# Kernel tuning notes

Measured on AMD Instinct MI355X. Metric: run time of the kernel, lower is better.

## Reference

```python
import jax, jax.numpy as jnp
import numpy as np

LAYERS, BLOCKS = 10, 4
RC, DC, SC, EC = 32, 32, 256, 256  # residual, dilation, skip, end channels
CIN, COUT, K = 6, 1, 2
DILATIONS = [2 ** (i % LAYERS) for i in range(BLOCKS * LAYERS)]
NL = len(DILATIONS)


def conv1d(x, w, dilation=1, pad=0):
    # x: [N, C, T], w: [O, I, K]
    return jax.lax.conv_general_dilated(
        x, w, window_strides=(1,), padding=[(pad, pad)],
        rhs_dilation=(dilation,), dimension_numbers=('NCH', 'OIH', 'NCH'))


def setup_inputs() -> dict:
    key = jax.random.key(0)
    ks = jax.random.split(key, 10)
    s = 0.1
    return {
        'x': jax.random.normal(ks[0], (8, CIN, 8192), dtype=jnp.float32),
        'start_w': jax.random.normal(ks[1], (RC, CIN, 1), dtype=jnp.float32) * s,
        'filter_w': jax.random.normal(ks[2], (NL, DC, RC, K), dtype=jnp.float32) * s,
        'gate_w': jax.random.normal(ks[3], (NL, DC, RC, K), dtype=jnp.float32) * s,
        'res_w': jax.random.normal(ks[4], (NL, RC, DC, 1), dtype=jnp.float32) * s,
        'skip_w': jax.random.normal(ks[5], (NL, SC, DC, 1), dtype=jnp.float32) * s,
        'end1_w': jax.random.normal(ks[6], (EC, SC, 1), dtype=jnp.float32) * s,
        'end1_b': jax.random.normal(ks[7], (EC,), dtype=jnp.float32) * s,
        'end2_w': jax.random.normal(ks[8], (COUT, EC, 1), dtype=jnp.float32) * s,
        'end2_b': jax.random.normal(ks[9], (COUT,), dtype=jnp.float32) * s,
    }


def reference(x, start_w, filter_w, gate_w, res_w, skip_w, end1_w, end1_b, end2_w, end2_b):
    x = conv1d(x, start_w)  # [B, RC, T]
    T = x.shape[2]
    # symmetric padding=(K-1)*d makes length grow by d each layer;
    # the shortest skip is the first one: T + (K-1)*DILATIONS[0]
    min_len = T + (K - 1) * DILATIONS[0]
    skip_sum = jnp.zeros((x.shape[0], SC, min_len), dtype=x.dtype)
    for i, d in enumerate(DILATIONS):
        pad = (K - 1) * d
        f = jnp.tanh(conv1d(x, filter_w[i], d, pad))
        g = jax.nn.sigmoid(conv1d(x, gate_w[i], d, pad))
        x = f * g  # [B, DC, T'] with T' = T_prev + d
        s = conv1d(x, skip_w[i])
        skip_sum = skip_sum + s[:, :, -min_len:]
        x = conv1d(x, res_w[i]) + x  # residual add (RC == DC)
    h = jax.nn.relu(skip_sum)
    h = jax.nn.relu(conv1d(h, end1_w) + end1_b[None, :, None])
    h = conv1d(h, end2_w) + end2_b[None, :, None]
    return h[:, :, -1]  # [B, COUT]
```

## Files before the change

kernel.cpp:

```cpp
#include <hip/hip_runtime.h>
#include <hip/hip_fp16.h>
#include <math.h>


#define NL 40
#define TLEN 8192

#define F_BLOBFG 0
#define F_BLOBSK 40960
#define F_BLOBE1 204800
#define F_C0     237568

typedef __attribute__((ext_vector_type(2))) _Float16 h2;

#if defined(__has_builtin)
#if __has_builtin(__builtin_amdgcn_fdot2)
#define HAS_FDOT2 1
#endif
#endif

__device__ __forceinline__ float FDOT2(h2 a, h2 b, float c) {
#ifdef HAS_FDOT2
    return __builtin_amdgcn_fdot2(a, b, c, false);
#else
    return c + (float)a.x * (float)b.x + (float)a.y * (float)b.y;
#endif
}

__device__ __forceinline__ float tanh_fast(float f) {
    f = fminf(fmaxf(f, -15.f), 15.f);
    float e2 = __expf(2.f * f);
    return (e2 - 1.f) / (e2 + 1.f);
}

__global__ __launch_bounds__(256) void k1_prep(
    const float* __restrict__ x, const float* __restrict__ start_w,
    const float* __restrict__ filter_w, const float* __restrict__ gate_w,
    const float* __restrict__ res_w, const float* __restrict__ skip_w,
    const float* __restrict__ end1_w, float* __restrict__ ws)
{
    const int id = blockIdx.x, t = threadIdx.x;

    if (id < 80) {
        const int l = id >> 1, m = id & 1;
        __shared__ float F[32][32];
        __shared__ __align__(16) float R[32][36];
        const float* src = m ? gate_w : filter_w;
        for (int e = t; e < 1024; e += 256)
            F[e >> 5][e & 31] = src[(l * 1024 + e) * 2];
        if (l > 0)
            for (int e = t; e < 1024; e += 256) {
                const int k = e >> 5, j = e & 31;
                R[k][j] = res_w[(l - 1) * 1024 + e] + (k == j ? 1.f : 0.f);
            }
        __syncthreads();
        const int ch = t >> 3, jg = t & 7, j0 = jg * 4;
        float o0, o1, o2, o3;
        if (l == 0) {
            o0 = F[ch][j0]; o1 = F[ch][j0+1]; o2 = F[ch][j0+2]; o3 = F[ch][j0+3];
        } else {
            o0 = o1 = o2 = o3 = 0.f;
#pragma unroll
            for (int k = 0; k < 32; ++k) {
                const float fv = F[ch][k];
                const float4 rv = *(const float4*)&R[k][j0];
                o0 += fv*rv.x; o1 += fv*rv.y; o2 += fv*rv.z; o3 += fv*rv.w;
            }
        }
        const int hh = jg >> 2;
        __half* dst = (__half*)ws + (size_t)l * 2048 + (hh * 32 + ch) * 32
                    + (m ? 16 : 0) + (j0 & 15);
        ((__half2*)dst)[0] = __floats2half2_rn(o0, o1);
        ((__half2*)dst)[1] = __floats2half2_rn(o2, o3);
    }
    else if (id == 80) {
        const int b = t >> 5, ch = t & 31;
        float acc = 0.f;
#pragma unroll
        for (int j = 0; j < 6; ++j)
            acc += start_w[ch * 6 + j] * x[(b * 6 + j) * TLEN + TLEN - 1];
        ws[F_C0 + t] = acc;
    }
    else if (id < 241) {
        const int q = (id - 81) * 256 + t;
        const float4* s4 = (const float4*)skip_w;
        const float4 a = s4[q * 2], bb = s4[q * 2 + 1];
        __half2* d = (__half2*)(ws + F_BLOBSK);
        d[q * 4 + 0] = __floats2half2_rn(a.x,  a.y);
        d[q * 4 + 1] = __floats2half2_rn(a.z,  a.w);
        d[q * 4 + 2] = __floats2half2_rn(bb.x, bb.y);
        d[q * 4 + 3] = __floats2half2_rn(bb.z, bb.w);
    }
    else {
        __half2* d = (__half2*)(ws + F_BLOBE1);
#pragma unroll
        for (int k = 0; k < 2; ++k) {
            const int dd = (id - 241) * 512 + k * 256 + t;
            const int ec = dd & 255, sc2 = dd >> 8;
            const float v0 = end1_w[ec * 256 + 2 * sc2];
            const float v1 = end1_w[ec * 256 + 2 * sc2 + 1];
            d[dd] = __floats2half2_rn(v0, v1);
        }
    }
}

#define PF(L, W) do {                                                        \
    if ((L) < NL) {                                                          \
        _Pragma("unroll")                                                    \
        for (int i = 0; i < 4; ++i)                                          \
            W[i] = blobfg[(L) * 256 + lane * 4 + i];                         \
    }                                                                        \
} while (0)

#define SPF(L, SW) do {                                                      \
    if ((L) < NL) {                                                          \
        _Pragma("unroll")                                                    \
        for (int i = 0; i < 4; ++i)                                          \
            SW[i] = blobsk[(L) * 1024 + sc * 4 + i];                         \
    }                                                                        \
} while (0)

#define BODY(L, FG, SW) do {                                                 \
    if (wv == 0) {                                                           \
        h2 s[8];                                                             \
        { const float4* sp = (const float4*)zown;                            \
          *(float4*)&s[0] = sp[h * 2];                                       \
          *(float4*)&s[4] = sp[h * 2 + 1]; }                                 \
        float f = 0.f, g = 0.f;                                              \
        const h2* wfp = (const h2*)&FG[0];                                   \
        const h2* wgp = (const h2*)&FG[2];                                   \
        _Pragma("unroll")                                                    \
        for (int i = 0; i < 8; ++i) {                                        \
            f = FDOT2(wfp[i], s[i], f);                                      \
            g = FDOT2(wgp[i], s[i], g);                                      \
        }                                                                    \
        f += __shfl_xor(f, 32, 64);                                          \
        g += __shfl_xor(g, 32, 64);                                          \
        const float z = tanh_fast(f) * (1.f / (1.f + __expf(-g)));           \
        const __half hz = __float2half(z);                                   \
        if (h == 0) { zown[ch] = hz; zring[(L) & 1][ch] = hz; }              \
        PF((L) + 4, FG);                                                     \
    } else {                                                                 \
        if ((L) >= 1) {                                                      \
            const h2* zr2 = (const h2*)zring[((L) - 1) & 1];                 \
            const h2* wp  = (const h2*)SW;                                   \
            _Pragma("unroll")                                                \
            for (int i = 0; i < 16; ++i)                                     \
                skip_acc = FDOT2(wp[i], zr2[i], skip_acc);                   \
        }                                                                    \
        SPF((L) + 1, SW);                                                    \
    }                                                                        \
    __syncthreads();                                                         \
} while (0)

__global__ __launch_bounds__(320) void k2_all(
    const float* __restrict__ end1_b, const float* __restrict__ end2_w,
    const float* __restrict__ end2_b, const float* __restrict__ ws,
    float* __restrict__ out)
{
    const int b = blockIdx.x, t = threadIdx.x;
    const int wv = t >> 6, lane = t & 63;
    const int ch = lane & 31, h = lane >> 5;
    const int sc = t - 64;

    __shared__ __align__(16) __half zown[32];
    __shared__ __align__(16) __half zring[2][32];
    __shared__ __align__(16) __half hhalf[256];
    __shared__ float psum[4];

    const float4* blobfg = (const float4*)ws;
    const float4* blobsk = (const float4*)(ws + F_BLOBSK);
    const h2*     blobe1 = (const h2*)(ws + F_BLOBE1);

    float4 fg0[4], fg1[4], fg2[4], fg3[4];
    float4 sw0[4], sw1[4];
    float skip_acc = 0.f, b1 = 0.f, w2 = 0.f;

    if (wv == 0) {
        if (h == 0) zown[ch] = __float2half(ws[F_C0 + b * 32 + ch]);
        PF(0, fg0); PF(1, fg1); PF(2, fg2); PF(3, fg3);
    } else {
        b1 = end1_b[sc];
        w2 = end2_w[sc];
        SPF(0, sw0);
    }
    __syncthreads();

    for (int l = 0; l < NL; l += 4) {
        BODY(l + 0, fg0, sw1);
        BODY(l + 1, fg1, sw0);
        BODY(l + 2, fg2, sw1);
        BODY(l + 3, fg3, sw0);
    }

    if (wv >= 1) {
        const h2* zr2 = (const h2*)zring[1];
        const h2* wp  = (const h2*)sw1;
#pragma unroll
        for (int i = 0; i < 16; ++i)
            skip_acc = FDOT2(wp[i], zr2[i], skip_acc);
        hhalf[sc] = __float2half(fmaxf(skip_acc, 0.f));
    }
    __syncthreads();

    if (wv >= 1) {
        float acc = b1;
        const h2* hh2 = (const h2*)hhalf;
#pragma unroll 8
        for (int s2 = 0; s2 < 128; ++s2)
            acc = FDOT2(blobe1[s2 * 256 + sc], hh2[s2], acc);
        float pe = fmaxf(acc, 0.f) * w2;
#pragma unroll
        for (int off = 32; off > 0; off >>= 1)
            pe += __shfl_down(pe, off, 64);
        if (lane == 0) psum[wv - 1] = pe;
    }
    __syncthreads();
    if (t == 64)
        out[b] = psum[0] + psum[1] + psum[2] + psum[3] + end2_b[0];
}

extern "C" void kernel_launch(void* const* d_in, const int* in_sizes, int n_in,
                              void* d_out, int out_size, void* d_ws, size_t ws_size,
                              hipStream_t stream) {
    const float* x        = (const float*)d_in[0];
    const float* start_w  = (const float*)d_in[1];
    const float* filter_w = (const float*)d_in[2];
    const float* gate_w   = (const float*)d_in[3];
    const float* res_w    = (const float*)d_in[4];
    const float* skip_w   = (const float*)d_in[5];
    const float* end1_w   = (const float*)d_in[6];
    const float* end1_b   = (const float*)d_in[7];
    const float* end2_w   = (const float*)d_in[8];
    const float* end2_b   = (const float*)d_in[9];
    float* out = (float*)d_out;
    float* ws  = (float*)d_ws;

    k1_prep<<<305, 256, 0, stream>>>(x, start_w, filter_w, gate_w, res_w,
                                     skip_w, end1_w, ws);
    k2_all <<<8, 320, 0, stream>>>(end1_b, end2_w, end2_b, ws, out);
}
```

Before: 106.9 us.

## Replace per-layer block barriers with producer-consumer flag and full z history

The gate wave now runs all 40 layers without block-wide barriers, writing each layer's z into a full-history shared buffer and publishing progress through a volatile shared counter. Skip-accumulating waves spin on that counter and consume each layer's z when it is ready, double-buffering their skip weights. This removes 40 __syncthreads per block so the serial recurrence on wave 0 is never stalled by the consumer waves. In exchange it adds busy-wait polling on LDS and relies on ordering between the z stores and the flag store without an explicit memory fence.

```diff
diff --git a/kernel.cpp b/kernel.cpp
--- a/kernel.cpp
+++ b/kernel.cpp
@@ -120,37 +120,41 @@
     }                                                                        \
 } while (0)
 
-#define BODY(L, FG, SW) do {                                                 \
-    if (wv == 0) {                                                           \
-        h2 s[8];                                                             \
-        { const float4* sp = (const float4*)zown;                            \
-          *(float4*)&s[0] = sp[h * 2];                                       \
-          *(float4*)&s[4] = sp[h * 2 + 1]; }                                 \
-        float f = 0.f, g = 0.f;                                              \
-        const h2* wfp = (const h2*)&FG[0];                                   \
-        const h2* wgp = (const h2*)&FG[2];                                   \
-        _Pragma("unroll")                                                    \
-        for (int i = 0; i < 8; ++i) {                                        \
-            f = FDOT2(wfp[i], s[i], f);                                      \
-            g = FDOT2(wgp[i], s[i], g);                                      \
-        }                                                                    \
-        f += __shfl_xor(f, 32, 64);                                          \
-        g += __shfl_xor(g, 32, 64);                                          \
-        const float z = tanh_fast(f) * (1.f / (1.f + __expf(-g)));           \
-        const __half hz = __float2half(z);                                   \
-        if (h == 0) { zown[ch] = hz; zring[(L) & 1][ch] = hz; }              \
-        PF((L) + 4, FG);                                                     \
-    } else {                                                                 \
-        if ((L) >= 1) {                                                      \
-            const h2* zr2 = (const h2*)zring[((L) - 1) & 1];                 \
-            const h2* wp  = (const h2*)SW;                                   \
-            _Pragma("unroll")                                                \
-            for (int i = 0; i < 16; ++i)                                     \
-                skip_acc = FDOT2(wp[i], zr2[i], skip_acc);                   \
-        }                                                                    \
-        SPF((L) + 1, SW);                                                    \
+#define K2_STEP(L, W) do {                                                   \
+    h2 s[8];                                                                 \
+    { const float4* sp = (const float4*)(zring + (L) * 32);                  \
+      *(float4*)&s[0] = sp[h * 2];                                           \
+      *(float4*)&s[4] = sp[h * 2 + 1]; }                                     \
+    float f = 0.f, g = 0.f;                                                  \
+    const h2* wfp = (const h2*)&W[0];                                        \
+    const h2* wgp = (const h2*)&W[2];                                        \
+    _Pragma("unroll")                                                        \
+    for (int i = 0; i < 8; ++i) {                                            \
+        f = FDOT2(wfp[i], s[i], f);                                          \
+        g = FDOT2(wgp[i], s[i], g);                                          \
     }                                                                        \
-    __syncthreads();                                                         \
+    f += __shfl_xor(f, 32, 64);                                              \
+    g += __shfl_xor(g, 32, 64);                                              \
+    const float z = tanh_fast(f) * (1.f / (1.f + __expf(-g)));               \
+    if (h == 0) zring[((L) + 1) * 32 + ch] = __float2half(z);                \
+    __builtin_amdgcn_wave_barrier();                                         \
+    if (lane == 0) *(volatile int*)&prog = (L) + 1;                          \
+    __builtin_amdgcn_wave_barrier();                                         \
+    PF((L) + 4, W);                                                          \
+} while (0)
+
+#define CSTEP(L, SW) do {                                                    \
+    while (*(volatile int*)&prog < (L) + 1) {}                               \
+    __builtin_amdgcn_wave_barrier();                                         \
+    h2 zz[16];                                                               \
+    { const float4* zp = (const float4*)(zring + ((L) + 1) * 32);            \
+      *(float4*)&zz[0]  = zp[0];  *(float4*)&zz[4]  = zp[1];                 \
+      *(float4*)&zz[8]  = zp[2];  *(float4*)&zz[12] = zp[3]; }               \
+    const h2* wp = (const h2*)SW;                                            \
+    _Pragma("unroll")                                                        \
+    for (int i = 0; i < 16; ++i)                                             \
+        skip_acc = FDOT2(wp[i], zz[i], skip_acc);                            \
+    SPF((L) + 2, SW);                                                        \
 } while (0)
 
 __global__ __launch_bounds__(320) void k2_all(
@@ -163,42 +167,40 @@
     const int ch = lane & 31, h = lane >> 5;
     const int sc = t - 64;
 
-    __shared__ __align__(16) __half zown[32];
-    __shared__ __align__(16) __half zring[2][32];
+    __shared__ __align__(16) __half zring[(NL + 1) * 32];
     __shared__ __align__(16) __half hhalf[256];
     __shared__ float psum[4];
+    __shared__ int prog;
 
     const float4* blobfg = (const float4*)ws;
     const float4* blobsk = (const float4*)(ws + F_BLOBSK);
     const h2*     blobe1 = (const h2*)(ws + F_BLOBE1);
 
-    float4 fg0[4], fg1[4], fg2[4], fg3[4];
-    float4 sw0[4], sw1[4];
-    float skip_acc = 0.f, b1 = 0.f, w2 = 0.f;
+    float b1 = 0.f, w2 = 0.f, skip_acc = 0.f;
+
+    if (wv == 0 && h == 0)
+        zring[ch] = __float2half(ws[F_C0 + b * 32 + ch]);
+    if (t == 0) *(volatile int*)&prog = 0;
+    __syncthreads();
 
     if (wv == 0) {
-        if (h == 0) zown[ch] = __float2half(ws[F_C0 + b * 32 + ch]);
+        float4 fg0[4], fg1[4], fg2[4], fg3[4];
         PF(0, fg0); PF(1, fg1); PF(2, fg2); PF(3, fg3);
+        for (int l = 0; l < NL; l += 4) {
+            K2_STEP(l + 0, fg0);
+            K2_STEP(l + 1, fg1);
+            K2_STEP(l + 2, fg2);
+            K2_STEP(l + 3, fg3);
+        }
     } else {
+        float4 swA[4], swB[4];
+        SPF(0, swA); SPF(1, swB);
         b1 = end1_b[sc];
         w2 = end2_w[sc];
-        SPF(0, sw0);
-    }
-    __syncthreads();
-
-    for (int l = 0; l < NL; l += 4) {
-        BODY(l + 0, fg0, sw1);
-        BODY(l + 1, fg1, sw0);
-        BODY(l + 2, fg2, sw1);
-        BODY(l + 3, fg3, sw0);
-    }
-
-    if (wv >= 1) {
-        const h2* zr2 = (const h2*)zring[1];
-        const h2* wp  = (const h2*)sw1;
-#pragma unroll
-        for (int i = 0; i < 16; ++i)
-            skip_acc = FDOT2(wp[i], zr2[i], skip_acc);
+        for (int l = 0; l < NL; l += 2) {
+            CSTEP(l + 0, swA);
+            CSTEP(l + 1, swB);
+        }
         hhalf[sc] = __float2half(fmaxf(skip_acc, 0.f));
     }
     __syncthreads();
```

Result: faster. 102.0 us (-4.5%).
